# Kernel tuning notes

Hardware: AMD Instinct MI355X
Metric: run time of the kernel (lower is better)

Reference implementation:

```python
import jax, jax.numpy as jnp
import numpy as np

B, N, C = 4, 2048, 768
H = 12
HD = C // H  # 64


def setup_inputs() -> dict:
    key = jax.random.key(0)
    ks = jax.random.split(key, 6)
    s = 0.02
    return {
        "x": jax.random.normal(ks[0], (B, N, C), dtype=jnp.float32),
        "w_qkv": jax.random.normal(ks[1], (C, 3 * C), dtype=jnp.float32) * s,
        "b_qkv": jax.random.normal(ks[2], (3 * C,), dtype=jnp.float32) * s,
        "w_proj": jax.random.normal(ks[3], (C, C), dtype=jnp.float32) * s,
        "b_proj": jax.random.normal(ks[4], (C,), dtype=jnp.float32) * s,
        "key_log_bias": jax.random.normal(ks[5], (B, N), dtype=jnp.float32),
    }


def reference(x, w_qkv, b_qkv, w_proj, b_proj, key_log_bias):
    b, n, c = x.shape
    scale = 1.0 / float(HD) ** 0.5
    qkv = x @ w_qkv + b_qkv                      # [B, N, 3C]
    qkv = qkv.reshape(b, n, 3, H, HD).transpose(2, 0, 3, 1, 4)  # [3, B, H, N, HD]
    q, k, v = qkv[0], qkv[1], qkv[2]
    logits = jnp.einsum('bhqd,bhkd->bhqk', q, k) * scale        # [B, H, N, N]
    logits = logits + key_log_bias[:, None, None, :]            # key-side bias
    attn = jax.nn.softmax(logits, axis=-1)
    out = jnp.einsum('bhqk,bhkd->bhqd', attn, v)                # [B, H, N, HD]
    out = out.transpose(0, 2, 1, 3).reshape(b, n, c)            # [B, N, C]
    return out @ w_proj + b_proj
```

## Files before the change

### kernel.cpp

```cpp
#include <hip/hip_runtime.h>


typedef short short8 __attribute__((ext_vector_type(8)));
typedef float f32x4 __attribute__((ext_vector_type(4)));
typedef unsigned int u32x4 __attribute__((ext_vector_type(4)));

#define GLB_AS(p) ((const __attribute__((address_space(1))) void*)(p))
#define LDS_AS(p) ((__attribute__((address_space(3))) void*)(p))

__device__ __forceinline__ void gload_lds16(const void* g, void* l) {
  __builtin_amdgcn_global_load_lds(GLB_AS(g), LDS_AS(l), 16, 0, 0);
}

__device__ __forceinline__ f32x4 mfma16(short8 a, short8 b, f32x4 c) {
  return __builtin_amdgcn_mfma_f32_16x16x32_bf16(a, b, c, 0, 0, 0);
}

__device__ __forceinline__ unsigned short f2bf(float f) {
  union { float f; unsigned u; } v; v.f = f;
  unsigned r = v.u + 0x7fffu + ((v.u >> 16) & 1u);
  return (unsigned short)(r >> 16);
}

__device__ __forceinline__ float bf2f(unsigned short u) {
  union { unsigned u; float f; } v; v.u = ((unsigned)u) << 16;
  return v.f;
}

__device__ __forceinline__ unsigned cvt_pk_bf16(float a, float b) {
  unsigned r;
  asm("v_cvt_pk_bf16_f32 %0, %1, %2" : "=v"(r) : "v"(a), "v"(b));
  return r;
}

#define LOG2E 1.44269504088896340736f

__device__ __forceinline__ int kappa1(int m) {
  return ((m >> 4) & 1) * 32 + ((m >> 2) & 3) * 8 + ((m >> 5) & 1) * 4 + (m & 3);
}


__global__ __launch_bounds__(256) void cvt_f32_bf16(const float* __restrict__ in,
                                                    unsigned short* __restrict__ out,
                                                    int n8) {
  int i = blockIdx.x * 256 + threadIdx.x;
  if (i >= n8) return;
  const float4* p = (const float4*)in + 2 * (size_t)i;
  float4 a = p[0], c = p[1];
  short8 r;
  r[0] = (short)f2bf(a.x); r[1] = (short)f2bf(a.y); r[2] = (short)f2bf(a.z); r[3] = (short)f2bf(a.w);
  r[4] = (short)f2bf(c.x); r[5] = (short)f2bf(c.y); r[6] = (short)f2bf(c.z); r[7] = (short)f2bf(c.w);
  ((short8*)out)[i] = r;
}

__global__ __launch_bounds__(256) void exp_bias(const float* __restrict__ in,
                                                unsigned short* __restrict__ out, int n) {
  int i = blockIdx.x * 256 + threadIdx.x;
  if (i < n) out[i] = f2bf(__builtin_exp2f(in[i] * LOG2E));
}

__global__ __launch_bounds__(256) void tr_cvt_f32_bf16(const float* __restrict__ src,
                                                       unsigned short* __restrict__ dst,
                                                       int R, int C) {
  __shared__ float t[32][33];
  int tx = threadIdx.x & 31, ty = threadIdx.x >> 5;
  int c0 = blockIdx.x * 32, r0 = blockIdx.y * 32;
#pragma unroll
  for (int i = 0; i < 32; i += 8)
    t[ty + i][tx] = src[(size_t)(r0 + ty + i) * C + c0 + tx];
  __syncthreads();
#pragma unroll
  for (int i = 0; i < 32; i += 8)
    dst[(size_t)(c0 + ty + i) * R + r0 + tx] = f2bf(t[tx][ty + i]);
}

__global__ __launch_bounds__(256) void tr_bf16_head(const unsigned short* __restrict__ src,
                                                    const unsigned short* __restrict__ ebb,
                                                    unsigned short* __restrict__ dst) {
  __shared__ unsigned short t[32][33];
  int tx = threadIdx.x & 31, ty = threadIdx.x >> 5;
  size_t hb = (size_t)blockIdx.z * (2048 * 64);
  int b = blockIdx.z / 12;
  int c0 = blockIdx.x * 32, r0 = blockIdx.y * 32;
#pragma unroll
  for (int i = 0; i < 32; i += 8)
    t[ty + i][tx] = src[hb + (size_t)(r0 + ty + i) * 64 + c0 + tx];
  __syncthreads();
  float eb = bf2f(ebb[b * 2048 + r0 + tx]);
#pragma unroll
  for (int i = 0; i < 32; i += 8)
    dst[hb + (size_t)(c0 + ty + i) * 2048 + r0 + tx] = f2bf(bf2f(t[tx][ty + i]) * eb);
}

template <int EPI>
__global__ __launch_bounds__(256, 2) void gemm_bt(
    const unsigned short* __restrict__ A, const unsigned short* __restrict__ Bt,
    const float* __restrict__ bias, float* __restrict__ outf,
    unsigned short* __restrict__ qo, unsigned short* __restrict__ ko,
    unsigned short* __restrict__ vo, int K) {
  __shared__ __align__(16) unsigned short As[128 * 64];
  __shared__ __align__(16) unsigned short Bs[128 * 64];
  const int tid = threadIdx.x;
  const int lane = tid & 63, wid = tid >> 6;
  const int lr = lane & 15, lg = lane >> 4;
  const int bm = blockIdx.x, bn = blockIdx.y;
  const int wr = (wid >> 1) * 64, wc = (wid & 1) * 64;

  const unsigned short* ap[4];
  const unsigned short* bp[4];
  unsigned loff[4];
#pragma unroll
  for (int i = 0; i < 4; ++i) {
    int c = wid * 4 + i;
    int r = c * 8 + (lane >> 3);
    int gs = (lane & 7) ^ (r & 7);
    ap[i] = A + (size_t)(bm * 128 + r) * K + gs * 8;
    bp[i] = Bt + (size_t)(bn * 128 + r) * K + gs * 8;
    loff[i] = (unsigned)c * 1024;
  }

  f32x4 acc[4][4] = {};
  const int nt = K >> 6;
  for (int t = 0; t < nt; ++t) {
#pragma unroll
    for (int i = 0; i < 4; ++i) {
      gload_lds16(ap[i], (char*)As + loff[i]);
      gload_lds16(bp[i], (char*)Bs + loff[i]);
      ap[i] += 64;
      bp[i] += 64;
    }
    __syncthreads();
#pragma unroll
    for (int kkk = 0; kkk < 2; ++kkk) {
      short8 af[4], bf[4];
#pragma unroll
      for (int mf = 0; mf < 4; ++mf) {
        int r = wr + mf * 16 + lr;
        int g = kkk * 4 + lg;
        af[mf] = *(const short8*)((const char*)As + r * 128 + ((g ^ (r & 7)) << 4));
      }
#pragma unroll
      for (int nf = 0; nf < 4; ++nf) {
        int r = wc + nf * 16 + lr;
        int g = kkk * 4 + lg;
        bf[nf] = *(const short8*)((const char*)Bs + r * 128 + ((g ^ (r & 7)) << 4));
      }
#pragma unroll
      for (int mf = 0; mf < 4; ++mf)
#pragma unroll
        for (int nf = 0; nf < 4; ++nf)
          acc[mf][nf] = mfma16(af[mf], bf[nf], acc[mf][nf]);
    }
    __syncthreads();
  }

  const int colbase = bn * 128 + wc;
  float bv[4];
#pragma unroll
  for (int nf = 0; nf < 4; ++nf) bv[nf] = bias[colbase + nf * 16 + lr];

  if constexpr (EPI == 0) {
#pragma unroll
    for (int nf = 0; nf < 4; ++nf) {
      int col = colbase + nf * 16 + lr;
      int which = col / 768;
      int rem = col - which * 768;
      int h = rem >> 6, d = rem & 63;
#pragma unroll
      for (int mf = 0; mf < 4; ++mf) {
#pragma unroll
        for (int j = 0; j < 4; ++j) {
          int row = bm * 128 + wr + mf * 16 + lg * 4 + j;
          int bb = row >> 11, nn = row & 2047;
          float v = acc[mf][nf][j] + bv[nf];
          size_t off = (((size_t)bb * 12 + h) * 2048 + nn) * 64 + d;
          if (which == 0)
            qo[off] = f2bf(v * (0.125f * LOG2E));
          else if (which == 1)
            ko[off] = f2bf(v);
          else
            vo[off] = f2bf(v);
        }
      }
    }
  } else {
#pragma unroll
    for (int mf = 0; mf < 4; ++mf) {
#pragma unroll
      for (int j = 0; j < 4; ++j) {
        int row = bm * 128 + wr + mf * 16 + lg * 4 + j;
#pragma unroll
        for (int nf = 0; nf < 4; ++nf) {
          int col = colbase + nf * 16 + lr;
          outf[(size_t)row * 768 + col] = acc[mf][nf][j] + bv[nf];
        }
      }
    }
  }
}

__global__ __launch_bounds__(256, 3) void attn_fused(
    const unsigned short* __restrict__ Q, const unsigned short* __restrict__ Kx,
    const unsigned short* __restrict__ Vt, const unsigned short* __restrict__ ebb,
    unsigned short* __restrict__ Ao) {
  __shared__ __align__(16) unsigned short Ks[2][64 * 64];
  __shared__ __align__(16) unsigned short Vs[2][64 * 64];
  const int tid = threadIdx.x, lane = tid & 63, wid = tid >> 6;
  const int lr = lane & 15, lg = lane >> 4;
  const int qb = blockIdx.x, bh = blockIdx.y;
  const int b = bh / 12, h = bh - b * 12;
  const size_t hoff = (size_t)bh * (2048 * 64);
  const unsigned short* Qh = Q + hoff;
  const unsigned short* Kh = Kx + hoff;
  const unsigned short* Vh = Vt + hoff;
  const unsigned short* ebh = ebb + b * 2048;

  short8 qf[2][2];
#pragma unroll
  for (int mf = 0; mf < 2; ++mf)
#pragma unroll
    for (int kkk = 0; kkk < 2; ++kkk) {
      int qr = qb * 128 + wid * 32 + mf * 16 + lr;
      qf[mf][kkk] = *(const short8*)(Qh + (size_t)qr * 64 + kkk * 32 + lg * 8);
    }

  const int c0 = wid * 2, c1 = wid * 2 + 1;
  const int r0s = c0 * 8 + (lane >> 3), r1s = c1 * 8 + (lane >> 3);
  const int g0 = (lane & 7) ^ (r0s & 7), g1 = (lane & 7) ^ (r1s & 7);
  const int k1r0 = kappa1(r0s), k1r1 = kappa1(r1s);

  f32x4 o[2][4] = {};
  f32x4 ol[2] = {};

#define STAGE(buf, t)                                                                  \
  do {                                                                                 \
    const int kt0_ = (t) * 64;                                                         \
    gload_lds16(Kh + (size_t)(kt0_ + k1r0) * 64 + g0 * 8, (char*)Ks[buf] + c0 * 1024); \
    gload_lds16(Kh + (size_t)(kt0_ + k1r1) * 64 + g1 * 8, (char*)Ks[buf] + c1 * 1024); \
    gload_lds16(Vh + (size_t)r0s * 2048 + kt0_ + g0 * 8, (char*)Vs[buf] + c0 * 1024);  \
    gload_lds16(Vh + (size_t)r1s * 2048 + kt0_ + g1 * 8, (char*)Vs[buf] + c1 * 1024);  \
  } while (0)

  STAGE(0, 0);
  int cur = 0;

  for (int t = 0; t < 32; ++t) {
    __syncthreads();
    if (t + 1 < 32) STAGE(cur ^ 1, t + 1);

    const int kt0 = t * 64;

    short8 ebf[2];
#pragma unroll
    for (int kkk = 0; kkk < 2; ++kkk)
      ebf[kkk] = *(const short8*)(ebh + kt0 + kkk * 32 + lg * 8);

    f32x4 s[4][2] = {};
#pragma unroll
    for (int kkk = 0; kkk < 2; ++kkk) {
      short8 kf[4];
#pragma unroll
      for (int nf = 0; nf < 4; ++nf) {
        int r = nf * 16 + lr, g = kkk * 4 + lg;
        kf[nf] = *(const short8*)((const char*)Ks[cur] + r * 128 + ((g ^ (r & 7)) << 4));
      }
#pragma unroll
      for (int nf = 0; nf < 4; ++nf)
#pragma unroll
        for (int mf = 0; mf < 2; ++mf)
          s[nf][mf] = mfma16(kf[nf], qf[mf][kkk], s[nf][mf]);
    }

#pragma unroll
    for (int nf = 0; nf < 4; ++nf)
#pragma unroll
      for (int mf = 0; mf < 2; ++mf)
#pragma unroll
        for (int j = 0; j < 4; ++j)
          s[nf][mf][j] = __builtin_exp2f(s[nf][mf][j]);

    short8 pa[2][2];
#pragma unroll
    for (int mf = 0; mf < 2; ++mf)
#pragma unroll
      for (int kkk = 0; kkk < 2; ++kkk) {
        u32x4 w;
        w[0] = cvt_pk_bf16(s[kkk][mf][0], s[kkk][mf][1]);
        w[1] = cvt_pk_bf16(s[kkk][mf][2], s[kkk][mf][3]);
        w[2] = cvt_pk_bf16(s[kkk + 2][mf][0], s[kkk + 2][mf][1]);
        w[3] = cvt_pk_bf16(s[kkk + 2][mf][2], s[kkk + 2][mf][3]);
        pa[mf][kkk] = __builtin_bit_cast(short8, w);
      }

#pragma unroll
    for (int kkk = 0; kkk < 2; ++kkk) {
      short8 vf[4];
#pragma unroll
      for (int nf = 0; nf < 4; ++nf) {
        int r = nf * 16 + lr, g = kkk * 4 + lg;
        vf[nf] = *(const short8*)((const char*)Vs[cur] + r * 128 + ((g ^ (r & 7)) << 4));
      }
#pragma unroll
      for (int mf = 0; mf < 2; ++mf) {
        ol[mf] = mfma16(pa[mf][kkk], ebf[kkk], ol[mf]);
#pragma unroll
        for (int nf = 0; nf < 4; ++nf)
          o[mf][nf] = mfma16(pa[mf][kkk], vf[nf], o[mf][nf]);
      }
    }
    cur ^= 1;
  }
#undef STAGE

#pragma unroll
  for (int mf = 0; mf < 2; ++mf)
#pragma unroll
    for (int j = 0; j < 4; ++j) {
      float inv = 1.f / ol[mf][j];
      int qr = qb * 128 + wid * 32 + mf * 16 + lg * 4 + j;
#pragma unroll
      for (int nf = 0; nf < 4; ++nf) {
        int d = nf * 16 + lr;
        Ao[((size_t)b * 2048 + qr) * 768 + h * 64 + d] = f2bf(o[mf][nf][j] * inv);
      }
    }
}


extern "C" void kernel_launch(void* const* d_in, const int* in_sizes, int n_in,
                              void* d_out, int out_size, void* d_ws, size_t ws_size,
                              hipStream_t stream) {
  (void)in_sizes; (void)n_in; (void)out_size; (void)ws_size;
  const float* x = (const float*)d_in[0];
  const float* wqkv = (const float*)d_in[1];
  const float* bqkv = (const float*)d_in[2];
  const float* wproj = (const float*)d_in[3];
  const float* bproj = (const float*)d_in[4];
  const float* klb = (const float*)d_in[5];
  float* out = (float*)d_out;
  char* ws = (char*)d_ws;

  const size_t SZ = (size_t)8192 * 768 * 2;
  unsigned short* xb = (unsigned short*)(ws);
  unsigned short* wqkvT = (unsigned short*)(ws + SZ);
  unsigned short* wprojT = (unsigned short*)(ws + SZ + 3538944);
  unsigned short* qbuf = (unsigned short*)(ws + SZ + 3538944 + 1179648);
  unsigned short* kbuf = (unsigned short*)(ws + SZ + 3538944 + 1179648 + SZ);
  unsigned short* vbuf = (unsigned short*)(ws + SZ + 3538944 + 1179648 + 2 * SZ);
  unsigned short* vtbuf = (unsigned short*)(ws + SZ + 3538944 + 1179648 + 3 * SZ);
  unsigned short* ebb = (unsigned short*)(ws + SZ + 3538944 + 1179648 + 4 * SZ);
  unsigned short* aob = xb;

  cvt_f32_bf16<<<dim3(3072), dim3(256), 0, stream>>>(x, xb, 786432);
  exp_bias<<<dim3(32), dim3(256), 0, stream>>>(klb, ebb, 8192);
  tr_cvt_f32_bf16<<<dim3(72, 24), dim3(256), 0, stream>>>(wqkv, wqkvT, 768, 2304);
  tr_cvt_f32_bf16<<<dim3(24, 24), dim3(256), 0, stream>>>(wproj, wprojT, 768, 768);
  gemm_bt<0><<<dim3(64, 18), dim3(256), 0, stream>>>(xb, wqkvT, bqkv, nullptr,
                                                     qbuf, kbuf, vbuf, 768);
  tr_bf16_head<<<dim3(2, 64, 48), dim3(256), 0, stream>>>(vbuf, ebb, vtbuf);
  attn_fused<<<dim3(16, 48), dim3(256), 0, stream>>>(qbuf, kbuf, vtbuf, ebb, aob);
  gemm_bt<1><<<dim3(64, 6), dim3(256), 0, stream>>>(aob, wprojT, bproj, out,
                                                    nullptr, nullptr, nullptr, 768);
}
```

Baseline: 158.5 us.

## Halve attention query tile and load V fragments directly from global

The attention kernel now handles 64 query rows per block instead of 128, so each wave processes one 16-row fragment and the grid doubles to 32x48 blocks. V is no longer staged through LDS: each lane reads its V^T fragments straight from global memory every key tile, and only K stays double-buffered in shared memory. Launch bounds rise to 4 blocks per CU. The aim is more blocks in flight, less LDS and fewer registers, at the cost of twice as many K/V reads across blocks and uncoalesced, unhidden global V loads inside the loop.

```diff
diff --git a/kernel.cpp b/kernel.cpp
--- a/kernel.cpp
+++ b/kernel.cpp
@@ -199,12 +199,11 @@
   }
 }
 
-__global__ __launch_bounds__(256, 3) void attn_fused(
+__global__ __launch_bounds__(256, 4) void attn_fused(
     const unsigned short* __restrict__ Q, const unsigned short* __restrict__ Kx,
     const unsigned short* __restrict__ Vt, const unsigned short* __restrict__ ebb,
     unsigned short* __restrict__ Ao) {
   __shared__ __align__(16) unsigned short Ks[2][64 * 64];
-  __shared__ __align__(16) unsigned short Vs[2][64 * 64];
   const int tid = threadIdx.x, lane = tid & 63, wid = tid >> 6;
   const int lr = lane & 15, lg = lane >> 4;
   const int qb = blockIdx.x, bh = blockIdx.y;
@@ -215,47 +214,54 @@
   const unsigned short* Vh = Vt + hoff;
   const unsigned short* ebh = ebb + b * 2048;
 
-  short8 qf[2][2];
-#pragma unroll
-  for (int mf = 0; mf < 2; ++mf)
-#pragma unroll
-    for (int kkk = 0; kkk < 2; ++kkk) {
-      int qr = qb * 128 + wid * 32 + mf * 16 + lr;
-      qf[mf][kkk] = *(const short8*)(Qh + (size_t)qr * 64 + kkk * 32 + lg * 8);
-    }
+  short8 qf[2];
+#pragma unroll
+  for (int kkk = 0; kkk < 2; ++kkk) {
+    int qr = qb * 64 + wid * 16 + lr;
+    qf[kkk] = *(const short8*)(Qh + (size_t)qr * 64 + kkk * 32 + lg * 8);
+  }
 
   const int c0 = wid * 2, c1 = wid * 2 + 1;
   const int r0s = c0 * 8 + (lane >> 3), r1s = c1 * 8 + (lane >> 3);
   const int g0 = (lane & 7) ^ (r0s & 7), g1 = (lane & 7) ^ (r1s & 7);
   const int k1r0 = kappa1(r0s), k1r1 = kappa1(r1s);
 
-  f32x4 o[2][4] = {};
-  f32x4 ol[2] = {};
-
-#define STAGE(buf, t)                                                                  \
+  const unsigned short* vp[4];
+#pragma unroll
+  for (int nf = 0; nf < 4; ++nf)
+    vp[nf] = Vh + (size_t)(nf * 16 + lr) * 2048 + lg * 8;
+
+  f32x4 o[4] = {};
+  f32x4 ol = {};
+
+#define STAGE_K(buf, t)                                                                \
   do {                                                                                 \
     const int kt0_ = (t) * 64;                                                         \
     gload_lds16(Kh + (size_t)(kt0_ + k1r0) * 64 + g0 * 8, (char*)Ks[buf] + c0 * 1024); \
     gload_lds16(Kh + (size_t)(kt0_ + k1r1) * 64 + g1 * 8, (char*)Ks[buf] + c1 * 1024); \
-    gload_lds16(Vh + (size_t)r0s * 2048 + kt0_ + g0 * 8, (char*)Vs[buf] + c0 * 1024);  \
-    gload_lds16(Vh + (size_t)r1s * 2048 + kt0_ + g1 * 8, (char*)Vs[buf] + c1 * 1024);  \
   } while (0)
 
-  STAGE(0, 0);
+  STAGE_K(0, 0);
   int cur = 0;
 
   for (int t = 0; t < 32; ++t) {
     __syncthreads();
-    if (t + 1 < 32) STAGE(cur ^ 1, t + 1);
+    if (t + 1 < 32) STAGE_K(cur ^ 1, t + 1);
 
     const int kt0 = t * 64;
 
+    short8 vr[4][2];
+#pragma unroll
+    for (int nf = 0; nf < 4; ++nf)
+#pragma unroll
+      for (int kkk = 0; kkk < 2; ++kkk)
+        vr[nf][kkk] = *(const short8*)(vp[nf] + kt0 + kkk * 32);
     short8 ebf[2];
 #pragma unroll
     for (int kkk = 0; kkk < 2; ++kkk)
       ebf[kkk] = *(const short8*)(ebh + kt0 + kkk * 32 + lg * 8);
 
-    f32x4 s[4][2] = {};
+    f32x4 s[4] = {};
 #pragma unroll
     for (int kkk = 0; kkk < 2; ++kkk) {
       short8 kf[4];
@@ -266,64 +272,47 @@
       }
 #pragma unroll
       for (int nf = 0; nf < 4; ++nf)
-#pragma unroll
-        for (int mf = 0; mf < 2; ++mf)
-          s[nf][mf] = mfma16(kf[nf], qf[mf][kkk], s[nf][mf]);
+        s[nf] = mfma16(kf[nf], qf[kkk], s[nf]);
     }
 
 #pragma unroll
     for (int nf = 0; nf < 4; ++nf)
 #pragma unroll
-      for (int mf = 0; mf < 2; ++mf)
-#pragma unroll
-        for (int j = 0; j < 4; ++j)
-          s[nf][mf][j] = __builtin_exp2f(s[nf][mf][j]);
-
-    short8 pa[2][2];
-#pragma unroll
-    for (int mf = 0; mf < 2; ++mf)
-#pragma unroll
-      for (int kkk = 0; kkk < 2; ++kkk) {
-        u32x4 w;
-        w[0] = cvt_pk_bf16(s[kkk][mf][0], s[kkk][mf][1]);
-        w[1] = cvt_pk_bf16(s[kkk][mf][2], s[kkk][mf][3]);
-        w[2] = cvt_pk_bf16(s[kkk + 2][mf][0], s[kkk + 2][mf][1]);
-        w[3] = cvt_pk_bf16(s[kkk + 2][mf][2], s[kkk + 2][mf][3]);
-        pa[mf][kkk] = __builtin_bit_cast(short8, w);
-      }
-
+      for (int j = 0; j < 4; ++j)
+        s[nf][j] = __builtin_exp2f(s[nf][j]);
+
+    short8 pa[2];
 #pragma unroll
     for (int kkk = 0; kkk < 2; ++kkk) {
-      short8 vf[4];
-#pragma unroll
-      for (int nf = 0; nf < 4; ++nf) {
-        int r = nf * 16 + lr, g = kkk * 4 + lg;
-        vf[nf] = *(const short8*)((const char*)Vs[cur] + r * 128 + ((g ^ (r & 7)) << 4));
-      }
-#pragma unroll
-      for (int mf = 0; mf < 2; ++mf) {
-        ol[mf] = mfma16(pa[mf][kkk], ebf[kkk], ol[mf]);
-#pragma unroll
-        for (int nf = 0; nf < 4; ++nf)
-          o[mf][nf] = mfma16(pa[mf][kkk], vf[nf], o[mf][nf]);
-      }
+      u32x4 w;
+      w[0] = cvt_pk_bf16(s[kkk][0], s[kkk][1]);
+      w[1] = cvt_pk_bf16(s[kkk][2], s[kkk][3]);
+      w[2] = cvt_pk_bf16(s[kkk + 2][0], s[kkk + 2][1]);
+      w[3] = cvt_pk_bf16(s[kkk + 2][2], s[kkk + 2][3]);
+      pa[kkk] = __builtin_bit_cast(short8, w);
+    }
+
+#pragma unroll
+    for (int kkk = 0; kkk < 2; ++kkk) {
+      ol = mfma16(pa[kkk], ebf[kkk], ol);
+#pragma unroll
+      for (int nf = 0; nf < 4; ++nf)
+        o[nf] = mfma16(pa[kkk], vr[nf][kkk], o[nf]);
     }
     cur ^= 1;
   }
-#undef STAGE
-
-#pragma unroll
-  for (int mf = 0; mf < 2; ++mf)
-#pragma unroll
-    for (int j = 0; j < 4; ++j) {
-      float inv = 1.f / ol[mf][j];
-      int qr = qb * 128 + wid * 32 + mf * 16 + lg * 4 + j;
-#pragma unroll
-      for (int nf = 0; nf < 4; ++nf) {
-        int d = nf * 16 + lr;
-        Ao[((size_t)b * 2048 + qr) * 768 + h * 64 + d] = f2bf(o[mf][nf][j] * inv);
-      }
-    }
+#undef STAGE_K
+
+#pragma unroll
+  for (int j = 0; j < 4; ++j) {
+    float inv = 1.f / ol[j];
+    int qr = qb * 64 + wid * 16 + lg * 4 + j;
+#pragma unroll
+    for (int nf = 0; nf < 4; ++nf) {
+      int d = nf * 16 + lr;
+      Ao[((size_t)b * 2048 + qr) * 768 + h * 64 + d] = f2bf(o[nf][j] * inv);
+    }
+  }
 }
 
 
@@ -358,7 +347,7 @@
   gemm_bt<0><<<dim3(64, 18), dim3(256), 0, stream>>>(xb, wqkvT, bqkv, nullptr,
                                                      qbuf, kbuf, vbuf, 768);
   tr_bf16_head<<<dim3(2, 64, 48), dim3(256), 0, stream>>>(vbuf, ebb, vtbuf);
-  attn_fused<<<dim3(16, 48), dim3(256), 0, stream>>>(qbuf, kbuf, vtbuf, ebb, aob);
+  attn_fused<<<dim3(32, 48), dim3(256), 0, stream>>>(qbuf, kbuf, vtbuf, ebb, aob);
   gemm_bt<1><<<dim3(64, 6), dim3(256), 0, stream>>>(aob, wprojT, bproj, out,
                                                     nullptr, nullptr, nullptr, 768);
 }
```

New measurement: 307.2 us. 93.8% more time.

## Load K/V fragments directly from global memory, dropping LDS staging and barriers

Applied to the files above, without the earlier changes.

The attention kernel no longer stages K and V tiles into double-buffered shared memory with async global-to-LDS loads and per-tile barriers. Each wave now reads its K and V MFMA fragments straight from global memory into registers, using precomputed per-lane pointers that keep the permuted K row order. This removes LDS traffic, the swizzle and the __syncthreads, but the four waves in a block now each fetch the same K/V data separately. It relies on L1/L2 caching to absorb that duplication, and there is no explicit prefetch left to hide load latency.

```diff
diff --git a/kernel.cpp b/kernel.cpp
--- a/kernel.cpp
+++ b/kernel.cpp
@@ -34,10 +34,6 @@
 }
 
 #define LOG2E 1.44269504088896340736f
-
-__device__ __forceinline__ int kappa1(int m) {
-  return ((m >> 4) & 1) * 32 + ((m >> 2) & 3) * 8 + ((m >> 5) & 1) * 4 + (m & 3);
-}
 
 
 __global__ __launch_bounds__(256) void cvt_f32_bf16(const float* __restrict__ in,
@@ -203,8 +199,6 @@
     const unsigned short* __restrict__ Q, const unsigned short* __restrict__ Kx,
     const unsigned short* __restrict__ Vt, const unsigned short* __restrict__ ebb,
     unsigned short* __restrict__ Ao) {
-  __shared__ __align__(16) unsigned short Ks[2][64 * 64];
-  __shared__ __align__(16) unsigned short Vs[2][64 * 64];
   const int tid = threadIdx.x, lane = tid & 63, wid = tid >> 6;
   const int lr = lane & 15, lg = lane >> 4;
   const int qb = blockIdx.x, bh = blockIdx.y;
@@ -224,32 +218,34 @@
       qf[mf][kkk] = *(const short8*)(Qh + (size_t)qr * 64 + kkk * 32 + lg * 8);
     }
 
-  const int c0 = wid * 2, c1 = wid * 2 + 1;
-  const int r0s = c0 * 8 + (lane >> 3), r1s = c1 * 8 + (lane >> 3);
-  const int g0 = (lane & 7) ^ (r0s & 7), g1 = (lane & 7) ^ (r1s & 7);
-  const int k1r0 = kappa1(r0s), k1r1 = kappa1(r1s);
+  const unsigned short* kp[4];
+  const unsigned short* vp[4];
+#pragma unroll
+  for (int nf = 0; nf < 4; ++nf) {
+    int krow = 32 * (nf & 1) + 4 * (nf >> 1) + 8 * (lr >> 2) + (lr & 3);
+    kp[nf] = Kh + (size_t)krow * 64 + lg * 8;
+    vp[nf] = Vh + (size_t)(nf * 16 + lr) * 2048 + lg * 8;
+  }
 
   f32x4 o[2][4] = {};
   f32x4 ol[2] = {};
 
-#define STAGE(buf, t)                                                                  \
-  do {                                                                                 \
-    const int kt0_ = (t) * 64;                                                         \
-    gload_lds16(Kh + (size_t)(kt0_ + k1r0) * 64 + g0 * 8, (char*)Ks[buf] + c0 * 1024); \
-    gload_lds16(Kh + (size_t)(kt0_ + k1r1) * 64 + g1 * 8, (char*)Ks[buf] + c1 * 1024); \
-    gload_lds16(Vh + (size_t)r0s * 2048 + kt0_ + g0 * 8, (char*)Vs[buf] + c0 * 1024);  \
-    gload_lds16(Vh + (size_t)r1s * 2048 + kt0_ + g1 * 8, (char*)Vs[buf] + c1 * 1024);  \
-  } while (0)
-
-  STAGE(0, 0);
-  int cur = 0;
-
   for (int t = 0; t < 32; ++t) {
-    __syncthreads();
-    if (t + 1 < 32) STAGE(cur ^ 1, t + 1);
-
     const int kt0 = t * 64;
 
+    short8 kf[4][2];
+#pragma unroll
+    for (int nf = 0; nf < 4; ++nf)
+#pragma unroll
+      for (int kkk = 0; kkk < 2; ++kkk)
+        kf[nf][kkk] = *(const short8*)(kp[nf] + (size_t)kt0 * 64 + kkk * 32);
+
+    short8 vr[4][2];
+#pragma unroll
+    for (int nf = 0; nf < 4; ++nf)
+#pragma unroll
+      for (int kkk = 0; kkk < 2; ++kkk)
+        vr[nf][kkk] = *(const short8*)(vp[nf] + kt0 + kkk * 32);
     short8 ebf[2];
 #pragma unroll
     for (int kkk = 0; kkk < 2; ++kkk)
@@ -257,19 +253,12 @@
 
     f32x4 s[4][2] = {};
 #pragma unroll
-    for (int kkk = 0; kkk < 2; ++kkk) {
-      short8 kf[4];
-#pragma unroll
-      for (int nf = 0; nf < 4; ++nf) {
-        int r = nf * 16 + lr, g = kkk * 4 + lg;
-        kf[nf] = *(const short8*)((const char*)Ks[cur] + r * 128 + ((g ^ (r & 7)) << 4));
-      }
+    for (int kkk = 0; kkk < 2; ++kkk)
 #pragma unroll
       for (int nf = 0; nf < 4; ++nf)
 #pragma unroll
         for (int mf = 0; mf < 2; ++mf)
-          s[nf][mf] = mfma16(kf[nf], qf[mf][kkk], s[nf][mf]);
-    }
+          s[nf][mf] = mfma16(kf[nf][kkk], qf[mf][kkk], s[nf][mf]);
 
 #pragma unroll
     for (int nf = 0; nf < 4; ++nf)
@@ -293,24 +282,15 @@
       }
 
 #pragma unroll
-    for (int kkk = 0; kkk < 2; ++kkk) {
-      short8 vf[4];
-#pragma unroll
-      for (int nf = 0; nf < 4; ++nf) {
-        int r = nf * 16 + lr, g = kkk * 4 + lg;
-        vf[nf] = *(const short8*)((const char*)Vs[cur] + r * 128 + ((g ^ (r & 7)) << 4));
-      }
+    for (int kkk = 0; kkk < 2; ++kkk)
 #pragma unroll
       for (int mf = 0; mf < 2; ++mf) {
         ol[mf] = mfma16(pa[mf][kkk], ebf[kkk], ol[mf]);
 #pragma unroll
         for (int nf = 0; nf < 4; ++nf)
-          o[mf][nf] = mfma16(pa[mf][kkk], vf[nf], o[mf][nf]);
-      }
-    }
-    cur ^= 1;
-  }
-#undef STAGE
+          o[mf][nf] = mfma16(pa[mf][kkk], vr[nf][kkk], o[mf][nf]);
+      }
+  }
 
 #pragma unroll
   for (int mf = 0; mf < 2; ++mf)
```

Result: slower. 258.4 us (+63.0%).
